# Kernel tuning notes

Measured on AMD Instinct MI355X. Metric: run time of the kernel, lower is better.

## Reference

```python
import jax, jax.numpy as jnp
import numpy as np

DIM = 1024
HEADS = 16
HEAD_DIM = DIM // HEADS
SCALE = HEAD_DIM ** -0.5


def setup_inputs() -> dict:
    key = jax.random.key(0)
    k1, k2, k3, k4 = jax.random.split(key, 4)
    x = jax.random.normal(k1, (8, 1024, DIM), dtype=jnp.float32)
    # nn.Linear weight is [out, in]; init ~ small values
    W_qkv = jax.random.normal(k2, (3 * DIM, DIM), dtype=jnp.float32) * 0.02
    W_proj = jax.random.normal(k3, (DIM, DIM), dtype=jnp.float32) * 0.02
    b_proj = jax.random.normal(k4, (DIM,), dtype=jnp.float32) * 0.02
    return {"x": x, "W_qkv": W_qkv, "W_proj": W_proj, "b_proj": b_proj}


def reference(x, W_qkv, W_proj, b_proj):
    b, n, _ = x.shape
    h, d = HEADS, HEAD_DIM
    qkv = x @ W_qkv.T  # [b, n, 3*dim]
    # rearrange 'b n (qkv h d) -> qkv b h n d'
    qkv = qkv.reshape(b, n, 3, h, d).transpose(2, 0, 3, 1, 4)
    q, k, v = qkv[0], qkv[1], qkv[2]  # each [b, h, n, d]
    dots = jnp.einsum('bhid,bhjd->bhij', q, k) * SCALE
    attn = jax.nn.softmax(dots, axis=-1)
    out = jnp.einsum('bhij,bhjd->bhid', attn, v)
    out = out.transpose(0, 2, 1, 3).reshape(b, n, h * d)  # b n (h d)
    return out @ W_proj.T + b_proj
```

## Files before the change

kernel.cpp:

```cpp
#include <hip/hip_runtime.h>
#include <math.h>

#define DIM   1024
#define HEADS 16
#define HDIM  64
#define SEQ   1024
#define BATCH 8
#define QSCALE 0.1803368801111204f
#define LDH   72
#define ABM   128

typedef __attribute__((ext_vector_type(8)))  short          short8_t;
typedef __attribute__((ext_vector_type(8)))  unsigned short ushort8_t;
typedef __attribute__((ext_vector_type(4)))  unsigned short ushort4_t;
typedef __attribute__((ext_vector_type(4)))  float          floatx4;
typedef __attribute__((ext_vector_type(16))) float          floatx16;

__device__ __forceinline__ unsigned short f2bf(float f) {
    unsigned u = __float_as_uint(f);
    u += 0x7fffu + ((u >> 16) & 1u);
    return (unsigned short)(u >> 16);
}
__device__ __forceinline__ unsigned rnd_bf(float f) {
    unsigned u = __float_as_uint(f);
    return u + 0x7fffu + ((u >> 16) & 1u);
}
__device__ __forceinline__ float fast_exp2(float x) {
#if __has_builtin(__builtin_amdgcn_exp2f)
    return __builtin_amdgcn_exp2f(x);
#else
    return exp2f(x);
#endif
}
__device__ __forceinline__ void glds16(const unsigned short* g, unsigned short* l) {
    __builtin_amdgcn_global_load_lds(
        (const __attribute__((address_space(1))) void*)g,
        (__attribute__((address_space(3))) void*)l, 16, 0, 0);
}

__global__ __launch_bounds__(256) void cvt_bf16_all(const float* __restrict__ x,
                                                    const float* __restrict__ wqkv,
                                                    const float* __restrict__ wproj,
                                                    unsigned short* __restrict__ x_o,
                                                    unsigned short* __restrict__ wqkv_o,
                                                    unsigned short* __restrict__ wproj_o) {
    const int N8_X = BATCH * SEQ * DIM / 8;
    const int N8_WQ = 3 * DIM * DIM / 8;
    const int N8_WP = DIM * DIM / 8;
    int i = blockIdx.x * 256 + threadIdx.x;
    const float* in;
    unsigned short* out;
    if (i < N8_X)               { in = x;     out = x_o; }
    else if (i < N8_X + N8_WQ)  { i -= N8_X;  in = wqkv; out = wqkv_o; }
    else                        { i -= N8_X + N8_WQ;
                                  if (i >= N8_WP) return;
                                  in = wproj; out = wproj_o; }
    const float4* p = (const float4*)in + (size_t)i * 2;
    float4 a = p[0], b = p[1];
    ushort8_t u;
    u[0] = f2bf(a.x); u[1] = f2bf(a.y); u[2] = f2bf(a.z); u[3] = f2bf(a.w);
    u[4] = f2bf(b.x); u[5] = f2bf(b.y); u[6] = f2bf(b.z); u[7] = f2bf(b.w);
    ((ushort8_t*)out)[i] = u;
}

template<int MODE>
__global__ __launch_bounds__(256) void gemm_nt_mfma(const unsigned short* __restrict__ A,
                                                    const unsigned short* __restrict__ B,
                                                    const float* __restrict__ bias,
                                                    void* __restrict__ Cout,
                                                    unsigned short* __restrict__ vt,
                                                    int M, int N, int K) {
    __shared__ __align__(16) unsigned short As[128 * 64];
    __shared__ __align__(16) unsigned short Bs[128 * 64];

    const int tid  = threadIdx.x;
    const int lane = tid & 63;
    const int wave = tid >> 6;
    const int wm = (wave >> 1) * 64;
    const int wn = (wave & 1) * 64;
    const size_t brow = (size_t)blockIdx.x * 128;
    const size_t bcol = (size_t)blockIdx.y * 128;

    const int srow   = lane >> 3;
    const int schunk = (lane & 7) ^ srow;
    const unsigned short* gA = A + (brow + wave * 8 + srow) * (size_t)K + schunk * 8;
    const unsigned short* gB = B + (bcol + wave * 8 + srow) * (size_t)K + schunk * 8;
    unsigned short* lA = &As[wave * 512 + lane * 8];
    unsigned short* lB = &Bs[wave * 512 + lane * 8];

    floatx16 acc[2][2];
    #pragma unroll
    for (int i = 0; i < 2; i++)
        #pragma unroll
        for (int j = 0; j < 2; j++)
            #pragma unroll
            for (int r = 0; r < 16; r++) acc[i][j][r] = 0.f;

    const int c32  = lane & 31;
    const int half = lane >> 5;
    const int xr   = c32 & 7;

    for (int k0 = 0; k0 < K; k0 += 64) {
        __syncthreads();
        #pragma unroll
        for (int r = 0; r < 4; r++) {
            glds16(gA + (size_t)r * 32 * K + k0, lA + r * 2048);
            glds16(gB + (size_t)r * 32 * K + k0, lB + r * 2048);
        }
        __syncthreads();

        #pragma unroll
        for (int s = 0; s < 4; s++) {
            const int ch = ((s * 2 + half) ^ xr) * 8;
            short8_t a0 = *(const short8_t*)&As[(wm + c32) * 64 + ch];
            short8_t a1 = *(const short8_t*)&As[(wm + 32 + c32) * 64 + ch];
            short8_t b0 = *(const short8_t*)&Bs[(wn + c32) * 64 + ch];
            short8_t b1 = *(const short8_t*)&Bs[(wn + 32 + c32) * 64 + ch];
            acc[0][0] = __builtin_amdgcn_mfma_f32_32x32x16_bf16(a0, b0, acc[0][0], 0, 0, 0);
            acc[0][1] = __builtin_amdgcn_mfma_f32_32x32x16_bf16(a0, b1, acc[0][1], 0, 0, 0);
            acc[1][0] = __builtin_amdgcn_mfma_f32_32x32x16_bf16(a1, b0, acc[1][0], 0, 0, 0);
            acc[1][1] = __builtin_amdgcn_mfma_f32_32x32x16_bf16(a1, b1, acc[1][1], 0, 0, 0);
        }
    }

    if (MODE == 0) {
        #pragma unroll
        for (int mi = 0; mi < 2; mi++)
            #pragma unroll
            for (int ni = 0; ni < 2; ni++) {
                const size_t col = bcol + wn + ni * 32 + c32;
                const float bv = bias[col];
                #pragma unroll
                for (int r = 0; r < 16; r++) {
                    const size_t row = brow + wm + mi * 32 + (r & 3) + 8 * (r >> 2) + 4 * half;
                    ((float*)Cout)[row * N + col] = acc[mi][ni][r] + bv;
                }
            }
    } else {
        if (bcol < 2048) {
            const float sc = (bcol < 1024) ? QSCALE : 1.0f;
            unsigned short* qk = (unsigned short*)Cout;
            #pragma unroll
            for (int mi = 0; mi < 2; mi++)
                #pragma unroll
                for (int ni = 0; ni < 2; ni++) {
                    const size_t col = bcol + wn + ni * 32 + c32;
                    #pragma unroll
                    for (int r = 0; r < 16; r++) {
                        const size_t row = brow + wm + mi * 32 + (r & 3) + 8 * (r >> 2) + 4 * half;
                        qk[row * 2048 + col] = f2bf(acc[mi][ni][r] * sc);
                    }
                }
        } else {
            #pragma unroll
            for (int mi = 0; mi < 2; mi++)
                #pragma unroll
                for (int ni = 0; ni < 2; ni++) {
                    const int dall = (int)(bcol + wn + ni * 32 + c32) - 2048;
                    const int h = dall >> 6, d = dall & 63;
                    #pragma unroll
                    for (int rg = 0; rg < 4; rg++) {
                        const size_t row0 = brow + wm + mi * 32 + rg * 8 + 4 * half;
                        const size_t bb = row0 >> 10;
                        const int n0 = (int)(row0 & 1023);
                        ushort4_t o;
                        #pragma unroll
                        for (int q = 0; q < 4; q++) o[q] = f2bf(acc[mi][ni][rg * 4 + q]);
                        *(ushort4_t*)&vt[(((size_t)bb * HEADS + h) * HDIM + d) * SEQ + n0] = o;
                    }
                }
        }
    }
}

__global__ __launch_bounds__(256) void attn_mfma(const unsigned short* __restrict__ qk,
                                                 const unsigned short* __restrict__ vt,
                                                 unsigned short* __restrict__ aout) {
    const int bh = blockIdx.x;
    const int qt = blockIdx.y;
    const int h  = bh & 15;
    const int b  = bh >> 4;
    const int tid  = threadIdx.x;
    const int lane = tid & 63;
    const int wave = tid >> 6;
    const int c32  = lane & 31;
    const int half = lane >> 5;

    __shared__ __align__(16) unsigned short Qs[ABM * LDH];
    __shared__ __align__(16) unsigned short Ks[2][64 * 64];
    __shared__ __align__(16) unsigned short Vs[2][64 * 64];
    __shared__ float scr[4][32];

    const int sr = tid >> 2;
    const int sq = tid & 3;
    const int sx = sr & 7;
    const unsigned short* ksrc0 =
        qk + ((size_t)(b * SEQ + sr)) * 2048 + DIM + h * HDIM + sq * 16;
    const unsigned short* vsrc0 =
        vt + (((size_t)(b * HEADS + h)) * HDIM + sr) * SEQ + sq * 16;
    const int kvo0 = sr * 64 + (((sq * 2)     ^ sx) * 8);
    const int kvo1 = sr * 64 + (((sq * 2 + 1) ^ sx) * 8);

    ushort8_t ck0 = *(const ushort8_t*)ksrc0;
    ushort8_t ck1 = *(const ushort8_t*)(ksrc0 + 8);
    ushort8_t cv0 = *(const ushort8_t*)vsrc0;
    ushort8_t cv1 = *(const ushort8_t*)(vsrc0 + 8);

    {
        const int r  = tid >> 1;
        const int c0 = (tid & 1) * 32;
        const unsigned short* src =
            qk + ((size_t)(b * SEQ + qt * ABM + r)) * 2048 + h * HDIM + c0;
        unsigned short* dst = &Qs[r * LDH + c0];
        *(ushort8_t*)(dst)      = *(const ushort8_t*)(src);
        *(ushort8_t*)(dst + 8)  = *(const ushort8_t*)(src + 8);
        *(ushort8_t*)(dst + 16) = *(const ushort8_t*)(src + 16);
        *(ushort8_t*)(dst + 24) = *(const ushort8_t*)(src + 24);
    }
    __syncthreads();

    short8_t bq[4];
    #pragma unroll
    for (int s = 0; s < 4; s++)
        bq[s] = *(const short8_t*)&Qs[(wave * 32 + c32) * LDH + s * 16 + half * 8];

    floatx16 O[2];
    #pragma unroll
    for (int dt = 0; dt < 2; dt++)
        #pragma unroll
        for (int r = 0; r < 16; r++) O[dt][r] = 0.f;
    float lsum = 0.f;

    const int fxr = c32 & 7;

    for (int kt = 0; kt < SEQ / 64; kt++) {
        const int cur = kt & 1;
        *(ushort8_t*)&Ks[cur][kvo0] = ck0;
        *(ushort8_t*)&Ks[cur][kvo1] = ck1;
        *(ushort8_t*)&Vs[cur][kvo0] = cv0;
        *(ushort8_t*)&Vs[cur][kvo1] = cv1;
        __syncthreads();
        if (kt + 1 < SEQ / 64) {
            const unsigned short* ks = ksrc0 + (size_t)(kt + 1) * 64 * 2048;
            const unsigned short* vs = vsrc0 + (kt + 1) * 64;
            ck0 = *(const ushort8_t*)ks;
            ck1 = *(const ushort8_t*)(ks + 8);
            cv0 = *(const ushort8_t*)vs;
            cv1 = *(const ushort8_t*)(vs + 8);
        }

        floatx16 S[2];
        #pragma unroll
        for (int t = 0; t < 2; t++)
            #pragma unroll
            for (int r = 0; r < 16; r++) S[t][r] = 0.f;
        #pragma unroll
        for (int t = 0; t < 2; t++)
            #pragma unroll
            for (int s = 0; s < 4; s++) {
                const int slot = ((s * 2 + half) ^ fxr) * 8;
                short8_t ak = *(const short8_t*)&Ks[cur][(t * 32 + c32) * 64 + slot];
                S[t] = __builtin_amdgcn_mfma_f32_32x32x16_bf16(ak, bq[s], S[t], 0, 0, 0);
            }

        #pragma unroll
        for (int t = 0; t < 2; t++)
            #pragma unroll
            for (int rg = 0; rg < 4; rg++) {
                const float p0 = fast_exp2(S[t][rg * 4 + 0]);
                const float p1 = fast_exp2(S[t][rg * 4 + 1]);
                const float p2 = fast_exp2(S[t][rg * 4 + 2]);
                const float p3 = fast_exp2(S[t][rg * 4 + 3]);
                lsum += (p0 + p1) + (p2 + p3);
                const unsigned r01 = __builtin_amdgcn_perm(rnd_bf(p1), rnd_bf(p0), 0x07060302);
                const unsigned r23 = __builtin_amdgcn_perm(rnd_bf(p3), rnd_bf(p2), 0x07060302);
                *(uint2*)&Qs[(wave * 32 + c32) * LDH + t * 32 + rg * 8 + 4 * half] =
                    make_uint2(r01, r23);
            }

        short8_t ap[4];
        #pragma unroll
        for (int s = 0; s < 4; s++)
            ap[s] = *(const short8_t*)&Qs[(wave * 32 + c32) * LDH + s * 16 + half * 8];
        #pragma unroll
        for (int dt = 0; dt < 2; dt++)
            #pragma unroll
            for (int s = 0; s < 4; s++) {
                const int slot = ((s * 2 + half) ^ fxr) * 8;
                short8_t bv = *(const short8_t*)&Vs[cur][(dt * 32 + c32) * 64 + slot];
                O[dt] = __builtin_amdgcn_mfma_f32_32x32x16_bf16(ap[s], bv, O[dt], 0, 0, 0);
            }
    }

    lsum += __shfl_xor(lsum, 32);
    if (half == 0) scr[wave][c32] = 1.0f / lsum;
    __builtin_amdgcn_s_waitcnt(0);

    #pragma unroll
    for (int rg = 0; rg < 4; rg++) {
        const float4 inv4 = *(const float4*)&scr[wave][rg * 8 + 4 * half];
        #pragma unroll
        for (int q = 0; q < 4; q++) {
            const float invl = ((const float*)&inv4)[q];
            const size_t row = (size_t)b * SEQ + qt * ABM + wave * 32 + rg * 8 + 4 * half + q;
            #pragma unroll
            for (int dt = 0; dt < 2; dt++)
                aout[row * DIM + h * HDIM + dt * 32 + c32] = f2bf(O[dt][rg * 4 + q] * invl);
        }
    }
}

extern "C" void kernel_launch(void* const* d_in, const int* in_sizes, int n_in,
                              void* d_out, int out_size, void* d_ws, size_t ws_size,
                              hipStream_t stream) {
    const float* x      = (const float*)d_in[0];
    const float* W_qkv  = (const float*)d_in[1];
    const float* W_proj = (const float*)d_in[2];
    const float* b_proj = (const float*)d_in[3];
    float* out = (float*)d_out;

    const int M = BATCH * SEQ;

    unsigned short* ws       = (unsigned short*)d_ws;
    unsigned short* x_bf     = ws;
    unsigned short* wqkv_bf  = x_bf + (size_t)M * DIM;
    unsigned short* wproj_bf = wqkv_bf + (size_t)3 * DIM * DIM;
    unsigned short* qk_bf    = wproj_bf + (size_t)DIM * DIM;
    unsigned short* vt_bf    = qk_bf + (size_t)M * 2048;
    unsigned short* aout_bf  = vt_bf + (size_t)BATCH * HEADS * HDIM * SEQ;

    {
        const int n8 = (M * DIM + 3 * DIM * DIM + DIM * DIM) / 8;
        cvt_bf16_all<<<(n8 + 255) / 256, 256, 0, stream>>>(
            x, W_qkv, W_proj, x_bf, wqkv_bf, wproj_bf);
    }

    gemm_nt_mfma<2><<<dim3(M / 128, 3 * DIM / 128), 256, 0, stream>>>(
        x_bf, wqkv_bf, nullptr, qk_bf, vt_bf, M, 3 * DIM, DIM);

    attn_mfma<<<dim3(BATCH * HEADS, SEQ / ABM), 256, 0, stream>>>(qk_bf, vt_bf, aout_bf);

    gemm_nt_mfma<0><<<dim3(M / 128, DIM / 128), 256, 0, stream>>>(
        aout_bf, wproj_bf, b_proj, out, nullptr, M, DIM, DIM);
}
```

Measured before the change: 237.8 us.

## Replace QKV GEMM with 256x256 eight-wave ping-pong pipelined MFMA kernel

Adds a dedicated QKV projection GEMM using 256x256 tiles, 512 threads, and direct global-to-LDS loads into double-buffered, XOR-swizzled shared memory. The main loop is split into phases that interleave staged loads with MFMA work, with explicit waitcnt, barriers and setprio. The aim is higher MFMA utilisation and better operand reuse than the previous 128x128 kernel. The cost is tightly hand-scheduled code hardcoded for K=1024 and these shapes, plus fewer, larger blocks.

```diff
diff --git a/kernel.cpp b/kernel.cpp
--- a/kernel.cpp
+++ b/kernel.cpp
@@ -173,6 +173,151 @@
     }
 }
 
+#define STG(t, part) do {                                                               \
+    const unsigned short* g_ = (((part) < 2) ? gA0 : gB0)                               \
+        + (size_t)(((part) & 1) * 128) * 1024 + (t) * 64;                               \
+    unsigned short* l_ = (((part) < 2) ? lA0 : lB0)                                     \
+        + ((t) & 1) * 16384 + ((part) & 1) * 8192;                                      \
+    glds16(g_, l_);                                                                     \
+    glds16(g_ + 64 * 1024, l_ + 4096);                                                  \
+} while (0)
+
+#define LDA(buf, mh) {                                                                  \
+    const unsigned short* p_ = AsF + (buf) * 16384 + aoff + (mh) * 4096;                \
+    a[0][0] = *(const short8_t*)(p_ + ch0);        a[0][1] = *(const short8_t*)(p_ + ch1); \
+    a[1][0] = *(const short8_t*)(p_ + 1024 + ch0); a[1][1] = *(const short8_t*)(p_ + 1024 + ch1); \
+    a[2][0] = *(const short8_t*)(p_ + 2048 + ch0); a[2][1] = *(const short8_t*)(p_ + 2048 + ch1); \
+    a[3][0] = *(const short8_t*)(p_ + 3072 + ch0); a[3][1] = *(const short8_t*)(p_ + 3072 + ch1); \
+}
+
+#define LDB(buf, nh) {                                                                  \
+    const unsigned short* p_ = BsF + (buf) * 16384 + boff + (nh) * 2048;                \
+    b[(nh)*2+0][0] = *(const short8_t*)(p_ + ch0);        b[(nh)*2+0][1] = *(const short8_t*)(p_ + ch1); \
+    b[(nh)*2+1][0] = *(const short8_t*)(p_ + 1024 + ch0); b[(nh)*2+1][1] = *(const short8_t*)(p_ + 1024 + ch1); \
+}
+
+#define MM(mh, nh) {                                                                    \
+    _Pragma("unroll")                                                                   \
+    for (int mf_ = 0; mf_ < 4; ++mf_) {                                                 \
+        _Pragma("unroll")                                                               \
+        for (int nf_ = 0; nf_ < 2; ++nf_) {                                             \
+            floatx4* c_ = &acc[(mh)*4+mf_][(nh)*2+nf_];                                 \
+            *c_ = __builtin_amdgcn_mfma_f32_16x16x32_bf16(a[mf_][0], b[(nh)*2+nf_][0], *c_, 0, 0, 0); \
+            *c_ = __builtin_amdgcn_mfma_f32_16x16x32_bf16(a[mf_][1], b[(nh)*2+nf_][1], *c_, 0, 0, 0); \
+        } } }
+
+#define PH_TAIL(mh, nh)                                                                 \
+    __builtin_amdgcn_s_barrier();                                                       \
+    asm volatile("s_waitcnt lgkmcnt(0)" ::: "memory");                                  \
+    __builtin_amdgcn_sched_barrier(0);                                                  \
+    __builtin_amdgcn_s_setprio(1);                                                      \
+    MM(mh, nh);                                                                         \
+    __builtin_amdgcn_s_setprio(0);                                                      \
+    __builtin_amdgcn_s_barrier();
+
+#define VM6 asm volatile("s_waitcnt vmcnt(6)" ::: "memory")
+#define VM0 asm volatile("s_waitcnt vmcnt(0)" ::: "memory")
+
+#define GROUP(buf, S1, S2, S3, S4, VMW)                                                 \
+    LDA(buf, 0); LDB(buf, 0); S1; PH_TAIL(0, 0);                                        \
+    LDB(buf, 1);              S2; PH_TAIL(0, 1);                                        \
+    LDA(buf, 1);              S3; PH_TAIL(1, 1);                                        \
+                              S4; VMW; PH_TAIL(1, 0);
+
+__global__ __launch_bounds__(512, 2) void gemm_qkv_8ph(const unsigned short* __restrict__ A,
+                                                       const unsigned short* __restrict__ B,
+                                                       unsigned short* __restrict__ qk,
+                                                       unsigned short* __restrict__ vt) {
+    __shared__ __align__(16) unsigned short As[2][16384];
+    __shared__ __align__(16) unsigned short Bs[2][16384];
+
+    const int tid  = threadIdx.x;
+    const int lane = tid & 63;
+    const int wave = tid >> 6;
+    const int wm   = wave >> 2;
+    const int wn   = wave & 3;
+    const size_t brow = (size_t)blockIdx.x * 256;
+    const size_t bcol = (size_t)blockIdx.y * 256;
+
+    const int ro  = tid >> 3;
+    const int lch = (tid & 7) ^ (ro & 7);
+    const unsigned short* gA0 = A + (brow + ro) * 1024 + lch * 8;
+    const unsigned short* gB0 = B + (bcol + ro) * 1024 + lch * 8;
+    unsigned short* lA0 = &As[0][0] + tid * 8;
+    unsigned short* lB0 = &Bs[0][0] + tid * 8;
+
+    const int l15  = lane & 15;
+    const int ch0  = (((lane >> 4)    ) ^ (lane & 7)) * 8;
+    const int ch1  = (((lane >> 4) + 4) ^ (lane & 7)) * 8;
+    const int aoff = (wm * 128 + l15) * 64;
+    const int boff = (wn * 64  + l15) * 64;
+    const unsigned short* AsF = &As[0][0];
+    const unsigned short* BsF = &Bs[0][0];
+
+    short8_t a[4][2];
+    short8_t b[4][2];
+    floatx4  acc[8][4];
+    #pragma unroll
+    for (int i = 0; i < 8; i++)
+        #pragma unroll
+        for (int j = 0; j < 4; j++)
+            #pragma unroll
+            for (int r = 0; r < 4; r++) acc[i][j][r] = 0.f;
+
+    STG(0, 3); STG(0, 0); STG(0, 1); STG(0, 2);
+    STG(1, 3); STG(1, 0); STG(1, 1);
+    VM6;
+    __builtin_amdgcn_s_barrier();
+
+    #pragma unroll 1
+    for (int i = 0; i < 7; ++i) {
+        GROUP(0, STG(2*i+1, 2), STG(2*i+2, 3), STG(2*i+2, 0), STG(2*i+2, 1), VM6);
+        GROUP(1, STG(2*i+2, 2), STG(2*i+3, 3), STG(2*i+3, 0), STG(2*i+3, 1), VM6);
+    }
+    GROUP(0, STG(15, 2), (void)0, (void)0, (void)0, VM0);
+    GROUP(1, (void)0,    (void)0, (void)0, (void)0, (void)0);
+
+    const int rq = (lane >> 4) << 2;
+    if (bcol < 2048) {
+        const float sc = (bcol < 1024) ? QSCALE : 1.0f;
+        #pragma unroll
+        for (int mf = 0; mf < 8; ++mf) {
+            const size_t row0 = brow + wm * 128 + mf * 16 + rq;
+            #pragma unroll
+            for (int nf = 0; nf < 4; ++nf) {
+                const size_t col = bcol + wn * 64 + nf * 16 + l15;
+                #pragma unroll
+                for (int q = 0; q < 4; ++q)
+                    qk[(row0 + q) * 2048 + col] = f2bf(acc[mf][nf][q] * sc);
+            }
+        }
+    } else {
+        #pragma unroll
+        for (int mf = 0; mf < 8; ++mf) {
+            const int row0 = (int)brow + wm * 128 + mf * 16 + rq;
+            const int bb = row0 >> 10, n0 = row0 & 1023;
+            #pragma unroll
+            for (int nf = 0; nf < 4; ++nf) {
+                const int dall = (int)bcol - 2048 + wn * 64 + nf * 16 + l15;
+                const int h = dall >> 6, d = dall & 63;
+                ushort4_t o;
+                #pragma unroll
+                for (int q = 0; q < 4; ++q) o[q] = f2bf(acc[mf][nf][q]);
+                *(ushort4_t*)&vt[(((size_t)bb * HEADS + h) * HDIM + d) * SEQ + n0] = o;
+            }
+        }
+    }
+}
+
+#undef STG
+#undef LDA
+#undef LDB
+#undef MM
+#undef PH_TAIL
+#undef VM6
+#undef VM0
+#undef GROUP
+
 __global__ __launch_bounds__(256) void attn_mfma(const unsigned short* __restrict__ qk,
                                                  const unsigned short* __restrict__ vt,
                                                  unsigned short* __restrict__ aout) {
@@ -335,8 +480,8 @@
             x, W_qkv, W_proj, x_bf, wqkv_bf, wproj_bf);
     }
 
-    gemm_nt_mfma<2><<<dim3(M / 128, 3 * DIM / 128), 256, 0, stream>>>(
-        x_bf, wqkv_bf, nullptr, qk_bf, vt_bf, M, 3 * DIM, DIM);
+    gemm_qkv_8ph<<<dim3(M / 256, 3 * DIM / 256), 512, 0, stream>>>(
+        x_bf, wqkv_bf, qk_bf, vt_bf);
 
     attn_mfma<<<dim3(BATCH * HEADS, SEQ / ABM), 256, 0, stream>>>(qk_bf, vt_bf, aout_bf);
 
```

After: 238.3 us. No clear change (+0.2%).

## Use permlane32 swap for P fragment and XCD-aware GEMM block swizzle

Applied to the files above, without the earlier changes.

In the attention kernel, the softmax probability tile is no longer written to LDS and read back as the A operand of the PV MFMA. The packed bf16 values stay in registers and are regrouped across wave halves with permlane32_swap, removing an LDS round trip and its wait from the inner loop. Separately, the GEMM kernel remaps block indices so that neighbouring tiles land on the same XCD, aiming for better L2 reuse. The swizzle assumes the grid dimensions divide evenly by 4 and 2, and the permlane ordering must match the MFMA operand layout.

```diff
diff --git a/kernel.cpp b/kernel.cpp
--- a/kernel.cpp
+++ b/kernel.cpp
@@ -13,6 +13,8 @@
 typedef __attribute__((ext_vector_type(8)))  short          short8_t;
 typedef __attribute__((ext_vector_type(8)))  unsigned short ushort8_t;
 typedef __attribute__((ext_vector_type(4)))  unsigned short ushort4_t;
+typedef __attribute__((ext_vector_type(2)))  unsigned int   uintx2;
+typedef __attribute__((ext_vector_type(4)))  unsigned int   uintx4;
 typedef __attribute__((ext_vector_type(4)))  float          floatx4;
 typedef __attribute__((ext_vector_type(16))) float          floatx16;
 
@@ -36,6 +38,15 @@
     __builtin_amdgcn_global_load_lds(
         (const __attribute__((address_space(1))) void*)g,
         (__attribute__((address_space(3))) void*)l, 16, 0, 0);
+}
+
+__device__ __forceinline__ void xcd_swizzle(int& bx, int& by) {
+    const int lin = blockIdx.y * gridDim.x + blockIdx.x;
+    const int cw  = gridDim.x >> 2;
+    const int chh = gridDim.y >> 1;
+    const int i   = lin >> 3;
+    bx = (lin & 3) * cw + i / chh;
+    by = ((lin >> 2) & 1) * chh + i % chh;
 }
 
 __global__ __launch_bounds__(256) void cvt_bf16_all(const float* __restrict__ x,
@@ -78,8 +89,10 @@
     const int wave = tid >> 6;
     const int wm = (wave >> 1) * 64;
     const int wn = (wave & 1) * 64;
-    const size_t brow = (size_t)blockIdx.x * 128;
-    const size_t bcol = (size_t)blockIdx.y * 128;
+    int bxi, byi;
+    xcd_swizzle(bxi, byi);
+    const size_t brow = (size_t)bxi * 128;
+    const size_t bcol = (size_t)byi * 128;
 
     const int srow   = lane >> 3;
     const int schunk = (lane & 7) ^ srow;
@@ -263,6 +276,7 @@
                 S[t] = __builtin_amdgcn_mfma_f32_32x32x16_bf16(ak, bq[s], S[t], 0, 0, 0);
             }
 
+        unsigned w0[8], w1[8];
         #pragma unroll
         for (int t = 0; t < 2; t++)
             #pragma unroll
@@ -272,16 +286,20 @@
                 const float p2 = fast_exp2(S[t][rg * 4 + 2]);
                 const float p3 = fast_exp2(S[t][rg * 4 + 3]);
                 lsum += (p0 + p1) + (p2 + p3);
-                const unsigned r01 = __builtin_amdgcn_perm(rnd_bf(p1), rnd_bf(p0), 0x07060302);
-                const unsigned r23 = __builtin_amdgcn_perm(rnd_bf(p3), rnd_bf(p2), 0x07060302);
-                *(uint2*)&Qs[(wave * 32 + c32) * LDH + t * 32 + rg * 8 + 4 * half] =
-                    make_uint2(r01, r23);
+                w0[t * 4 + rg] = __builtin_amdgcn_perm(rnd_bf(p1), rnd_bf(p0), 0x07060302);
+                w1[t * 4 + rg] = __builtin_amdgcn_perm(rnd_bf(p3), rnd_bf(p2), 0x07060302);
             }
 
         short8_t ap[4];
         #pragma unroll
-        for (int s = 0; s < 4; s++)
-            ap[s] = *(const short8_t*)&Qs[(wave * 32 + c32) * LDH + s * 16 + half * 8];
+        for (int s = 0; s < 4; s++) {
+            uintx2 q0 = __builtin_amdgcn_permlane32_swap(w0[2 * s], w0[2 * s + 1], false, false);
+            uintx2 q1 = __builtin_amdgcn_permlane32_swap(w1[2 * s], w1[2 * s + 1], false, false);
+            uintx4 v;
+            v[0] = q0[0]; v[1] = q1[0]; v[2] = q0[1]; v[3] = q1[1];
+            ap[s] = *(short8_t*)&v;
+        }
+
         #pragma unroll
         for (int dt = 0; dt < 2; dt++)
             #pragma unroll
```

Result: no change. 236.6 us (-0.5%).
